# Optimization experiments

Measured on AMD Instinct MI355X. Metric: run time of the kernel, lower is better.

## Reference

```python
import jax, jax.numpy as jnp
import numpy as np

N_NODES = 100000
HIDDEN = 256
N_EDGES = 3200000


def _sage_conv(h, src, dst, Wl, bl, Wr, n_nodes):
    # PyG SAGEConv (aggr='mean', root_weight=True):
    #   out_i = Wl @ mean_{j in N(i)} h_j + bl + Wr @ h_i
    msgs = h[src]                                            # [E, D] gather
    summed = jax.ops.segment_sum(msgs, dst, num_segments=n_nodes)   # [N, D]
    deg = jax.ops.segment_sum(jnp.ones((src.shape[0],), h.dtype), dst,
                              num_segments=n_nodes)
    mean = summed / jnp.maximum(deg, 1.0)[:, None]
    return mean @ Wl.T + bl + h @ Wr.T


def _prelu(x, a):
    return jnp.where(x >= 0, x, a * x)


def setup_inputs() -> dict:
    key = jax.random.key(0)
    ks = jax.random.split(key, 16)
    D = HIDDEN
    s = 1.0 / np.sqrt(D)
    inp = {
        "x": jnp.arange(N_NODES, dtype=jnp.int64),
        "edge_index": jax.random.randint(ks[0], (2, N_EDGES), 0, N_NODES, dtype=jnp.int64),
        "edge_weight": jax.random.uniform(ks[1], (N_EDGES,), dtype=jnp.float32),
        "emb": jax.random.normal(ks[2], (N_NODES, D), dtype=jnp.float32),
    }
    i = 3
    for layer in (1, 2, 3):
        inp[f"Wl{layer}"] = jax.random.uniform(ks[i], (D, D), jnp.float32, -s, s); i += 1
        inp[f"bl{layer}"] = jax.random.uniform(ks[i], (D,), jnp.float32, -s, s); i += 1
        inp[f"Wr{layer}"] = jax.random.uniform(ks[i], (D, D), jnp.float32, -s, s); i += 1
        inp[f"a{layer}"] = jnp.array(0.25, jnp.float32)  # PReLU init
    inp["Wout"] = jax.random.uniform(ks[i], (D, D), jnp.float32, -s, s); i += 1
    inp["bout"] = jax.random.uniform(ks[i], (D,), jnp.float32, -s, s)
    return inp


def reference(x, edge_index, edge_weight, emb,
              Wl1, bl1, Wr1, a1,
              Wl2, bl2, Wr2, a2,
              Wl3, bl3, Wr3, a3,
              Wout, bout):
    # edge_weight is accepted but unused (original forward never passes it to SAGEConv).
    # Dropout treated as identity (eval mode) for a deterministic reference.
    n = emb.shape[0]
    src, dst = edge_index[0], edge_index[1]
    h0 = emb[x]                                              # embedding lookup
    h1 = _prelu(_sage_conv(h0, src, dst, Wl1, bl1, Wr1, n), a1)
    h2 = _prelu(_sage_conv(h1, src, dst, Wl2, bl2, Wr2, n), a2)
    h3 = _prelu(_sage_conv(h2, src, dst, Wl3, bl3, Wr3, n), a3)
    return h3 @ Wout.T + bout
```

## Files before the change

### kernel.cpp

```cpp
#include <hip/hip_runtime.h>

#define D 256
typedef unsigned short u16;
using short8  = __attribute__((ext_vector_type(8))) short;
using ushort8 = __attribute__((ext_vector_type(8))) unsigned short;
using f32x4   = __attribute__((ext_vector_type(4))) float;

#define BCHUNK  4096
#define FBINCAP 17500

__device__ __forceinline__ u16 f2bf(float f) {
    unsigned u = __float_as_uint(f);
    unsigned r = (u + 0x7FFFu + ((u >> 16) & 1u)) >> 16;
    return (u16)r;
}
__device__ __forceinline__ float bf2f(u16 v) {
    return __uint_as_float(((unsigned)v) << 16);
}

__device__ __forceinline__ void load_lds16(const u16* g, u16* l) {
    __builtin_amdgcn_global_load_lds(
        (const __attribute__((address_space(1))) void*)g,
        (__attribute__((address_space(3))) void*)l, 16, 0, 0);
}


__global__ void k_initcur(int* __restrict__ bincur, int nfbin) {
    int i = threadIdx.x;
    if (i < nfbin) bincur[i] = i * FBINCAP;
}

__global__ __launch_bounds__(256)
void k_binf(const int* __restrict__ src, const int* __restrict__ dst,
            int* __restrict__ bincur, unsigned* __restrict__ bins,
            int E, int nfbin) {
    __shared__ int cnt[256];
    __shared__ int bpos[256];
    int t = threadIdx.x;
    int base = blockIdx.x * BCHUNK;
    cnt[t] = 0;
    __syncthreads();
    int lim = E - base; if (lim > BCHUNK) lim = BCHUNK;
    for (int i = t; i < lim; i += 256)
        atomicAdd(&cnt[dst[base + i] >> 9], 1);
    __syncthreads();
    if (t < nfbin) {
        int c = cnt[t];
        bpos[t] = c > 0 ? atomicAdd(&bincur[t], c) : 0;
    }
    __syncthreads();
    cnt[t] = 0;
    __syncthreads();
    for (int i = t; i < lim; i += 256) {
        int d = dst[base + i], s = src[base + i];
        int fb = d >> 9;
        int r = atomicAdd(&cnt[fb], 1);
        bins[(size_t)bpos[fb] + r] = (unsigned)s | ((unsigned)(d & 511) << 17);
    }
}

__global__ __launch_bounds__(256)
void k_csrf(const unsigned* __restrict__ bins, const int* __restrict__ bincur,
            int* __restrict__ offs, int* __restrict__ ends,
            int* __restrict__ srcs, int N) {
    __shared__ int cnt[512];
    __shared__ int cur[512];
    __shared__ int ssum[256];
    __shared__ int loc[FBINCAP];
    int b = blockIdx.x, t = threadIdx.x;
    int bbase = b * FBINCAP;
    int ecnt = bincur[b] - bbase;
    cnt[t] = 0; cnt[t + 256] = 0;
    __syncthreads();
    const unsigned* bp = bins + bbase;
    for (int i = t; i < ecnt; i += 256)
        atomicAdd(&cnt[bp[i] >> 17], 1);
    __syncthreads();
    int a0 = cnt[2 * t], a1 = cnt[2 * t + 1];
    ssum[t] = a0 + a1;
    __syncthreads();
    for (int o = 1; o < 256; o <<= 1) {
        int x = (t >= o) ? ssum[t - o] : 0;
        __syncthreads();
        ssum[t] += x;
        __syncthreads();
    }
    int excl = ssum[t] - (a0 + a1);
    cur[2 * t] = excl;
    cur[2 * t + 1] = excl + a0;
    int nbase = b << 9;
    int l0 = nbase + 2 * t, l1 = l0 + 1;
    if (l0 < N) { offs[l0] = bbase + excl;      ends[l0] = bbase + excl + a0; }
    if (l1 < N) { offs[l1] = bbase + excl + a0; ends[l1] = bbase + excl + a0 + a1; }
    __syncthreads();
    for (int i = t; i < ecnt; i += 256) {
        unsigned v = bp[i];
        int p = atomicAdd(&cur[v >> 17], 1);
        loc[p] = (int)(v & 0x1FFFFu);
    }
    __syncthreads();
    for (int i = t; i < ecnt; i += 256)
        srcs[bbase + i] = loc[i];
}


__global__ void k_gather_bf(const int* __restrict__ x, const float* __restrict__ emb,
                            u16* __restrict__ h, int N) {
    int idx = blockIdx.x * blockDim.x + threadIdx.x;
    if (idx >= N * 64) return;
    int node = idx >> 6, c = idx & 63;
    int s = x[node];
    float4 v = ((const float4*)emb)[(size_t)s * 64 + c];
    ushort4 o;
    o.x = f2bf(v.x); o.y = f2bf(v.y); o.z = f2bf(v.z); o.w = f2bf(v.w);
    ((ushort4*)h)[(size_t)node * 64 + c] = o;
}


__global__ void k_cvtw(const float* w0, const float* w1, const float* w2,
                       const float* w3, const float* w4, const float* w5,
                       const float* w6, u16* __restrict__ out) {
    int idx = blockIdx.x * blockDim.x + threadIdx.x;
    if (idx >= 7 * 65536) return;
    int m = idx >> 16, off = idx & 65535;
    const float* w = w0;
    if (m == 1) w = w1; else if (m == 2) w = w2; else if (m == 3) w = w3;
    else if (m == 4) w = w4; else if (m == 5) w = w5; else if (m == 6) w = w6;
    out[idx] = f2bf(w[off]);
}


__global__ void k_agg_half(const u16* __restrict__ h, const int* __restrict__ offs,
                           const int* __restrict__ ends, const int* __restrict__ srcs,
                           u16* __restrict__ out, int colOff, int N) {
    int wid = (blockIdx.x * blockDim.x + threadIdx.x) >> 6;
    int lane = threadIdx.x & 63;
    if (wid >= N) return;
    int beg = offs[wid], end = ends[wid];
    int q = lane >> 4;
    int cl = lane & 15;
    const u16* hb = h + colOff + cl * 8;
    float acc[8];
    #pragma unroll
    for (int i = 0; i < 8; i++) acc[i] = 0.f;
    int e = beg + q;
    for (; e + 12 < end; e += 16) {
        int j0 = srcs[e], j1 = srcs[e + 4], j2 = srcs[e + 8], j3 = srcs[e + 12];
        ushort8 v0 = *(const ushort8*)&hb[(size_t)j0 * D];
        ushort8 v1 = *(const ushort8*)&hb[(size_t)j1 * D];
        ushort8 v2 = *(const ushort8*)&hb[(size_t)j2 * D];
        ushort8 v3 = *(const ushort8*)&hb[(size_t)j3 * D];
        #pragma unroll
        for (int i = 0; i < 8; i++)
            acc[i] += (bf2f(v0[i]) + bf2f(v1[i])) + (bf2f(v2[i]) + bf2f(v3[i]));
    }
    for (; e < end; e += 4) {
        int j = srcs[e];
        ushort8 v = *(const ushort8*)&hb[(size_t)j * D];
        #pragma unroll
        for (int i = 0; i < 8; i++) acc[i] += bf2f(v[i]);
    }
    #pragma unroll
    for (int i = 0; i < 8; i++) {
        acc[i] += __shfl_xor(acc[i], 16);
        acc[i] += __shfl_xor(acc[i], 32);
    }
    if (q == 0) {
        int dg = end - beg;
        float inv = 1.0f / (float)(dg < 1 ? 1 : dg);
        ushort8 o;
        #pragma unroll
        for (int i = 0; i < 8; i++) o[i] = f2bf(acc[i] * inv);
        *(ushort8*)&out[(size_t)wid * D + colOff + cl * 8] = o;
    }
}


__global__ __launch_bounds__(512)
void k_fgemm(const u16* __restrict__ A0, const u16* __restrict__ W0,
             const u16* __restrict__ A1, const u16* __restrict__ W1,
             int npairs,
             const float* __restrict__ bias, const float* __restrict__ prelu_a,
             void* __restrict__ outp, int out_bf16, int M) {
    __shared__ u16 As[128 * 32];
    __shared__ u16 Bs[256 * 32];
    int t = threadIdx.x;
    int wave = t >> 6, lane = t & 63;
    int r = lane & 15, quad = lane >> 4;
    int wm = (wave & 1) * 64;
    int wn = (wave >> 1) * 64;
    int m0 = blockIdx.x * 128;

    f32x4 acc[4][4];
    #pragma unroll
    for (int i = 0; i < 4; i++)
        #pragma unroll
        for (int j = 0; j < 4; j++)
            acc[i][j] = (f32x4){0.f, 0.f, 0.f, 0.f};

    int rowA  = t >> 2,           colA  = (t & 3) * 8;
    int rowB1 = (t + 512) >> 2;
    u16* ldsA  = &As[wave * 512];
    u16* ldsB0 = &Bs[wave * 512];
    u16* ldsB1 = &Bs[4096 + wave * 512];

    for (int p = 0; p < npairs; ++p) {
        const u16* Ag = p ? A1 : A0;
        const u16* Wg = p ? W1 : W0;
        for (int kt = 0; kt < 8; ++kt) {
            int k0 = kt * 32;
            __syncthreads();
            load_lds16(Ag + (size_t)(m0 + rowA) * D + k0 + colA, ldsA);
            load_lds16(Wg + (size_t)rowA * D + k0 + colA, ldsB0);
            load_lds16(Wg + (size_t)rowB1 * D + k0 + colA, ldsB1);
            __syncthreads();

            short8 a[4], b[4];
            #pragma unroll
            for (int mt = 0; mt < 4; mt++)
                a[mt] = *(const short8*)&As[(wm + mt * 16 + r) * 32 + quad * 8];
            #pragma unroll
            for (int nt = 0; nt < 4; nt++)
                b[nt] = *(const short8*)&Bs[(wn + nt * 16 + r) * 32 + quad * 8];
            #pragma unroll
            for (int mt = 0; mt < 4; mt++)
                #pragma unroll
                for (int nt = 0; nt < 4; nt++)
                    acc[mt][nt] = __builtin_amdgcn_mfma_f32_16x16x32_bf16(
                        a[mt], b[nt], acc[mt][nt], 0, 0, 0);
        }
    }

    float pa = prelu_a ? *prelu_a : 0.f;
    int dop = prelu_a != nullptr;
    #pragma unroll
    for (int nt = 0; nt < 4; nt++) {
        int col = wn + nt * 16 + r;
        float bv = bias ? bias[col] : 0.f;
        #pragma unroll
        for (int mt = 0; mt < 4; mt++) {
            #pragma unroll
            for (int i = 0; i < 4; i++) {
                int row = m0 + wm + mt * 16 + quad * 4 + i;
                if (row < M) {
                    float v = acc[mt][nt][i] + bv;
                    if (dop) v = (v >= 0.f) ? v : pa * v;
                    if (out_bf16)
                        ((u16*)outp)[(size_t)row * D + col] = f2bf(v);
                    else
                        ((float*)outp)[(size_t)row * D + col] = v;
                }
            }
        }
    }
}


extern "C" void kernel_launch(void* const* d_in, const int* in_sizes, int n_in,
                              void* d_out, int out_size, void* d_ws, size_t ws_size,
                              hipStream_t stream) {
    const int*   x    = (const int*)d_in[0];
    const int*   ei   = (const int*)d_in[1];
    const float* emb  = (const float*)d_in[3];
    const float* Wl[3] = {(const float*)d_in[4],  (const float*)d_in[8],  (const float*)d_in[12]};
    const float* bl[3] = {(const float*)d_in[5],  (const float*)d_in[9],  (const float*)d_in[13]};
    const float* Wr[3] = {(const float*)d_in[6],  (const float*)d_in[10], (const float*)d_in[14]};
    const float* pa[3] = {(const float*)d_in[7],  (const float*)d_in[11], (const float*)d_in[15]};
    const float* Wout = (const float*)d_in[16];
    const float* bout = (const float*)d_in[17];

    int N = in_sizes[0];
    int E = in_sizes[1] / 2;
    const int* src = ei;
    const int* dst = ei + E;
    int nfbin = (N + 511) >> 9;

    char* ws = (char*)d_ws;
    size_t off = 0;
    auto walloc = [&](size_t bytes) -> void* {
        void* p = ws + off;
        off += (bytes + 255) & ~(size_t)255;
        return p;
    };
    u16* hA   = (u16*)walloc((size_t)N * D * sizeof(u16));
    u16* hB   = (u16*)walloc((size_t)N * D * sizeof(u16));
    u16* mean = (u16*)walloc((size_t)N * D * sizeof(u16));
    u16* wbf  = (u16*)walloc((size_t)7 * 65536 * sizeof(u16));
    int* offs   = (int*)walloc((size_t)N * sizeof(int));
    int* ends   = (int*)walloc((size_t)N * sizeof(int));
    int* bincur = (int*)walloc(1024);
    unsigned* bins = (unsigned*)walloc((size_t)nfbin * FBINCAP * sizeof(unsigned));
    int* srcs   = (int*)walloc((size_t)nfbin * FBINCAP * sizeof(int));

    u16* Wlb[3] = {wbf + 0 * 65536, wbf + 2 * 65536, wbf + 4 * 65536};
    u16* Wrb[3] = {wbf + 1 * 65536, wbf + 3 * 65536, wbf + 5 * 65536};
    u16* Woutb  = wbf + 6 * 65536;

    k_cvtw<<<(7 * 65536 + 255) / 256, 256, 0, stream>>>(
        Wl[0], Wr[0], Wl[1], Wr[1], Wl[2], Wr[2], Wout, wbf);

    k_initcur<<<1, 256, 0, stream>>>(bincur, nfbin);
    int bb = (E + BCHUNK - 1) / BCHUNK;
    k_binf<<<bb, 256, 0, stream>>>(src, dst, bincur, bins, E, nfbin);
    k_csrf<<<nfbin, 256, 0, stream>>>(bins, bincur, offs, ends, srcs, N);

    k_gather_bf<<<(N * 64 + 255) / 256, 256, 0, stream>>>(x, emb, hA, N);

    int mb   = (N + 127) / 128;
    int aggb = (N + 3) / 4;

    k_agg_half<<<aggb, 256, 0, stream>>>(hA, offs, ends, srcs, mean, 0, N);
    k_agg_half<<<aggb, 256, 0, stream>>>(hA, offs, ends, srcs, mean, 128, N);
    k_fgemm<<<mb, 512, 0, stream>>>(mean, Wlb[0], hA, Wrb[0], 2, bl[0], pa[0], hB, 1, N);
    k_agg_half<<<aggb, 256, 0, stream>>>(hB, offs, ends, srcs, mean, 0, N);
    k_agg_half<<<aggb, 256, 0, stream>>>(hB, offs, ends, srcs, mean, 128, N);
    k_fgemm<<<mb, 512, 0, stream>>>(mean, Wlb[1], hB, Wrb[1], 2, bl[1], pa[1], hA, 1, N);
    k_agg_half<<<aggb, 256, 0, stream>>>(hA, offs, ends, srcs, mean, 0, N);
    k_agg_half<<<aggb, 256, 0, stream>>>(hA, offs, ends, srcs, mean, 128, N);
    k_fgemm<<<mb, 512, 0, stream>>>(mean, Wlb[2], hA, Wrb[2], 2, bl[2], pa[2], hB, 1, N);
    k_fgemm<<<mb, 512, 0, stream>>>(hB, Woutb, hB, Woutb, 1, bout, nullptr, d_out, 0, N);
}
```

Before: 1.159 ms.

## Merge half-column aggregation passes and double-buffer GEMM with swizzled LDS tiles

Measured after the change: 1.283 ms. 1.11x slower.

```diff
diff --git a/kernel.cpp b/kernel.cpp
--- a/kernel.cpp
+++ b/kernel.cpp
@@ -130,22 +130,23 @@
 }
 
 
-__global__ void k_agg_half(const u16* __restrict__ h, const int* __restrict__ offs,
-                           const int* __restrict__ ends, const int* __restrict__ srcs,
-                           u16* __restrict__ out, int colOff, int N) {
+__global__ __launch_bounds__(256)
+void k_agg(const u16* __restrict__ h, const int* __restrict__ offs,
+           const int* __restrict__ ends, const int* __restrict__ srcs,
+           u16* __restrict__ out, int N) {
     int wid = (blockIdx.x * blockDim.x + threadIdx.x) >> 6;
     int lane = threadIdx.x & 63;
     if (wid >= N) return;
     int beg = offs[wid], end = ends[wid];
-    int q = lane >> 4;
-    int cl = lane & 15;
-    const u16* hb = h + colOff + cl * 8;
+    int q = lane >> 5;
+    int cl = lane & 31;
+    const u16* hb = h + cl * 8;
     float acc[8];
     #pragma unroll
     for (int i = 0; i < 8; i++) acc[i] = 0.f;
     int e = beg + q;
-    for (; e + 12 < end; e += 16) {
-        int j0 = srcs[e], j1 = srcs[e + 4], j2 = srcs[e + 8], j3 = srcs[e + 12];
+    for (; e + 6 < end; e += 8) {
+        int j0 = srcs[e], j1 = srcs[e + 2], j2 = srcs[e + 4], j3 = srcs[e + 6];
         ushort8 v0 = *(const ushort8*)&hb[(size_t)j0 * D];
         ushort8 v1 = *(const ushort8*)&hb[(size_t)j1 * D];
         ushort8 v2 = *(const ushort8*)&hb[(size_t)j2 * D];
@@ -154,36 +155,33 @@
         for (int i = 0; i < 8; i++)
             acc[i] += (bf2f(v0[i]) + bf2f(v1[i])) + (bf2f(v2[i]) + bf2f(v3[i]));
     }
-    for (; e < end; e += 4) {
+    for (; e < end; e += 2) {
         int j = srcs[e];
         ushort8 v = *(const ushort8*)&hb[(size_t)j * D];
         #pragma unroll
         for (int i = 0; i < 8; i++) acc[i] += bf2f(v[i]);
     }
     #pragma unroll
-    for (int i = 0; i < 8; i++) {
-        acc[i] += __shfl_xor(acc[i], 16);
-        acc[i] += __shfl_xor(acc[i], 32);
-    }
+    for (int i = 0; i < 8; i++) acc[i] += __shfl_xor(acc[i], 32);
     if (q == 0) {
         int dg = end - beg;
         float inv = 1.0f / (float)(dg < 1 ? 1 : dg);
         ushort8 o;
         #pragma unroll
         for (int i = 0; i < 8; i++) o[i] = f2bf(acc[i] * inv);
-        *(ushort8*)&out[(size_t)wid * D + colOff + cl * 8] = o;
-    }
-}
-
-
-__global__ __launch_bounds__(512)
+        *(ushort8*)&out[(size_t)wid * D + cl * 8] = o;
+    }
+}
+
+
+__global__ __launch_bounds__(512, 2)
 void k_fgemm(const u16* __restrict__ A0, const u16* __restrict__ W0,
              const u16* __restrict__ A1, const u16* __restrict__ W1,
              int npairs,
              const float* __restrict__ bias, const float* __restrict__ prelu_a,
              void* __restrict__ outp, int out_bf16, int M) {
-    __shared__ u16 As[128 * 32];
-    __shared__ u16 Bs[256 * 32];
+    __shared__ u16 As[2][128 * 64];
+    __shared__ u16 Bs[2][256 * 64];
     int t = threadIdx.x;
     int wave = t >> 6, lane = t & 63;
     int r = lane & 15, quad = lane >> 4;
@@ -198,37 +196,68 @@
         for (int j = 0; j < 4; j++)
             acc[i][j] = (f32x4){0.f, 0.f, 0.f, 0.f};
 
-    int rowA  = t >> 2,           colA  = (t & 3) * 8;
-    int rowB1 = (t + 512) >> 2;
-    u16* ldsA  = &As[wave * 512];
-    u16* ldsB0 = &Bs[wave * 512];
-    u16* ldsB1 = &Bs[4096 + wave * 512];
-
-    for (int p = 0; p < npairs; ++p) {
-        const u16* Ag = p ? A1 : A0;
-        const u16* Wg = p ? W1 : W0;
-        for (int kt = 0; kt < 8; ++kt) {
-            int k0 = kt * 32;
-            __syncthreads();
-            load_lds16(Ag + (size_t)(m0 + rowA) * D + k0 + colA, ldsA);
-            load_lds16(Wg + (size_t)rowA * D + k0 + colA, ldsB0);
-            load_lds16(Wg + (size_t)rowB1 * D + k0 + colA, ldsB1);
-            __syncthreads();
-
-            short8 a[4], b[4];
+    int l8   = lane >> 3;
+    int cb   = (lane & 7) * 16;
+    int scol = (cb ^ (l8 << 4)) >> 1;
+    int arow = wave * 8 + l8;
+
+    int nkt = npairs * 4;
+
+    auto STAGE = [&](int buf, int kt) {
+        const u16* Ag = (kt >= 4) ? A1 : A0;
+        const u16* Wg = (kt >= 4) ? W1 : W0;
+        int k0 = (kt & 3) * 64;
+        #pragma unroll
+        for (int l = 0; l < 2; l++) {
+            int row = l * 64 + arow;
+            load_lds16(Ag + (size_t)(m0 + row) * D + k0 + scol,
+                       &As[buf][l * 4096 + wave * 512]);
+        }
+        #pragma unroll
+        for (int l = 0; l < 4; l++) {
+            int row = l * 64 + arow;
+            load_lds16(Wg + (size_t)row * D + k0 + scol,
+                       &Bs[buf][l * 4096 + wave * 512]);
+        }
+    };
+
+    STAGE(0, 0);
+    __syncthreads();
+
+    int cur = 0;
+    for (int kt = 0; kt < nkt; ++kt) {
+        if (kt + 1 < nkt) STAGE(cur ^ 1, kt + 1);
+
+        short8 a[2][4], b[2][4];
+        #pragma unroll
+        for (int ks = 0; ks < 2; ks++) {
             #pragma unroll
-            for (int mt = 0; mt < 4; mt++)
-                a[mt] = *(const short8*)&As[(wm + mt * 16 + r) * 32 + quad * 8];
+            for (int mt = 0; mt < 4; mt++) {
+                int row = wm + mt * 16 + r;
+                int col = (ks * 64 + quad * 16) ^ ((r & 7) << 4);
+                a[ks][mt] = *(const short8*)&As[cur][row * 64 + (col >> 1)];
+            }
             #pragma unroll
-            for (int nt = 0; nt < 4; nt++)
-                b[nt] = *(const short8*)&Bs[(wn + nt * 16 + r) * 32 + quad * 8];
+            for (int nt = 0; nt < 4; nt++) {
+                int row = wn + nt * 16 + r;
+                int col = (ks * 64 + quad * 16) ^ ((r & 7) << 4);
+                b[ks][nt] = *(const short8*)&Bs[cur][row * 64 + (col >> 1)];
+            }
+        }
+
+        __builtin_amdgcn_s_setprio(1);
+        #pragma unroll
+        for (int ks = 0; ks < 2; ks++)
             #pragma unroll
             for (int mt = 0; mt < 4; mt++)
                 #pragma unroll
                 for (int nt = 0; nt < 4; nt++)
                     acc[mt][nt] = __builtin_amdgcn_mfma_f32_16x16x32_bf16(
-                        a[mt], b[nt], acc[mt][nt], 0, 0, 0);
-        }
+                        a[ks][mt], b[ks][nt], acc[mt][nt], 0, 0, 0);
+        __builtin_amdgcn_s_setprio(0);
+
+        __syncthreads();
+        cur ^= 1;
     }
 
     float pa = prelu_a ? *prelu_a : 0.f;
@@ -307,16 +336,13 @@
     k_gather_bf<<<(N * 64 + 255) / 256, 256, 0, stream>>>(x, emb, hA, N);
 
     int mb   = (N + 127) / 128;
-    int aggb = (N + 3) / 4;
-
-    k_agg_half<<<aggb, 256, 0, stream>>>(hA, offs, ends, srcs, mean, 0, N);
-    k_agg_half<<<aggb, 256, 0, stream>>>(hA, offs, ends, srcs, mean, 128, N);
+    int aggb = (N * 64 + 255) / 256;
+
+    k_agg<<<aggb, 256, 0, stream>>>(hA, offs, ends, srcs, mean, N);
     k_fgemm<<<mb, 512, 0, stream>>>(mean, Wlb[0], hA, Wrb[0], 2, bl[0], pa[0], hB, 1, N);
-    k_agg_half<<<aggb, 256, 0, stream>>>(hB, offs, ends, srcs, mean, 0, N);
-    k_agg_half<<<aggb, 256, 0, stream>>>(hB, offs, ends, srcs, mean, 128, N);
+    k_agg<<<aggb, 256, 0, stream>>>(hB, offs, ends, srcs, mean, N);
     k_fgemm<<<mb, 512, 0, stream>>>(mean, Wlb[1], hB, Wrb[1], 2, bl[1], pa[1], hA, 1, N);
-    k_agg_half<<<aggb, 256, 0, stream>>>(hA, offs, ends, srcs, mean, 0, N);
-    k_agg_half<<<aggb, 256, 0, stream>>>(hA, offs, ends, srcs, mean, 128, N);
+    k_agg<<<aggb, 256, 0, stream>>>(hA, offs, ends, srcs, mean, N);
     k_fgemm<<<mb, 512, 0, stream>>>(mean, Wlb[2], hA, Wrb[2], 2, bl[2], pa[2], hB, 1, N);
     k_fgemm<<<mb, 512, 0, stream>>>(hB, Woutb, hB, Woutb, 1, bout, nullptr, d_out, 0, N);
 }
```

## Triple-buffer GEMM LDS loads with swizzle; split first-layer aggregation into quarters

Applied to the files above, without the earlier changes.

After: 1.179 ms. About the same (+1.7%).

```diff
diff --git a/kernel.cpp b/kernel.cpp
--- a/kernel.cpp
+++ b/kernel.cpp
@@ -130,9 +130,10 @@
 }
 
 
-__global__ void k_agg_half(const u16* __restrict__ h, const int* __restrict__ offs,
-                           const int* __restrict__ ends, const int* __restrict__ srcs,
-                           u16* __restrict__ out, int colOff, int N) {
+__global__ __launch_bounds__(256)
+void k_agg_h(const u16* __restrict__ h, const int* __restrict__ offs,
+             const int* __restrict__ ends, const int* __restrict__ srcs,
+             u16* __restrict__ out, int colOff, int N) {
     int wid = (blockIdx.x * blockDim.x + threadIdx.x) >> 6;
     int lane = threadIdx.x & 63;
     if (wid >= N) return;
@@ -176,14 +177,62 @@
 }
 
 
-__global__ __launch_bounds__(512)
+__global__ __launch_bounds__(256)
+void k_agg_q(const u16* __restrict__ h, const int* __restrict__ offs,
+             const int* __restrict__ ends, const int* __restrict__ srcs,
+             u16* __restrict__ out, int colOff, int N) {
+    int wid = (blockIdx.x * blockDim.x + threadIdx.x) >> 6;
+    int lane = threadIdx.x & 63;
+    if (wid >= N) return;
+    int beg = offs[wid], end = ends[wid];
+    int q = lane >> 3;
+    int cl = lane & 7;
+    const u16* hb = h + colOff + cl * 8;
+    float acc[8];
+    #pragma unroll
+    for (int i = 0; i < 8; i++) acc[i] = 0.f;
+    int e = beg + q;
+    for (; e + 24 < end; e += 32) {
+        int j0 = srcs[e], j1 = srcs[e + 8], j2 = srcs[e + 16], j3 = srcs[e + 24];
+        ushort8 v0 = *(const ushort8*)&hb[(size_t)j0 * D];
+        ushort8 v1 = *(const ushort8*)&hb[(size_t)j1 * D];
+        ushort8 v2 = *(const ushort8*)&hb[(size_t)j2 * D];
+        ushort8 v3 = *(const ushort8*)&hb[(size_t)j3 * D];
+        #pragma unroll
+        for (int i = 0; i < 8; i++)
+            acc[i] += (bf2f(v0[i]) + bf2f(v1[i])) + (bf2f(v2[i]) + bf2f(v3[i]));
+    }
+    for (; e < end; e += 8) {
+        int j = srcs[e];
+        ushort8 v = *(const ushort8*)&hb[(size_t)j * D];
+        #pragma unroll
+        for (int i = 0; i < 8; i++) acc[i] += bf2f(v[i]);
+    }
+    #pragma unroll
+    for (int i = 0; i < 8; i++) {
+        acc[i] += __shfl_xor(acc[i], 8);
+        acc[i] += __shfl_xor(acc[i], 16);
+        acc[i] += __shfl_xor(acc[i], 32);
+    }
+    if (q == 0) {
+        int dg = end - beg;
+        float inv = 1.0f / (float)(dg < 1 ? 1 : dg);
+        ushort8 o;
+        #pragma unroll
+        for (int i = 0; i < 8; i++) o[i] = f2bf(acc[i] * inv);
+        *(ushort8*)&out[(size_t)wid * D + colOff + cl * 8] = o;
+    }
+}
+
+
+__global__ __launch_bounds__(512, 4)
 void k_fgemm(const u16* __restrict__ A0, const u16* __restrict__ W0,
              const u16* __restrict__ A1, const u16* __restrict__ W1,
              int npairs,
              const float* __restrict__ bias, const float* __restrict__ prelu_a,
              void* __restrict__ outp, int out_bf16, int M) {
-    __shared__ u16 As[128 * 32];
-    __shared__ u16 Bs[256 * 32];
+    __shared__ u16 As[3][128 * 32];
+    __shared__ u16 Bs[3][256 * 32];
     int t = threadIdx.x;
     int wave = t >> 6, lane = t & 63;
     int r = lane & 15, quad = lane >> 4;
@@ -198,37 +247,54 @@
         for (int j = 0; j < 4; j++)
             acc[i][j] = (f32x4){0.f, 0.f, 0.f, 0.f};
 
-    int rowA  = t >> 2,           colA  = (t & 3) * 8;
-    int rowB1 = (t + 512) >> 2;
-    u16* ldsA  = &As[wave * 512];
-    u16* ldsB0 = &Bs[wave * 512];
-    u16* ldsB1 = &Bs[4096 + wave * 512];
-
-    for (int p = 0; p < npairs; ++p) {
-        const u16* Ag = p ? A1 : A0;
-        const u16* Wg = p ? W1 : W0;
-        for (int kt = 0; kt < 8; ++kt) {
-            int k0 = kt * 32;
-            __syncthreads();
-            load_lds16(Ag + (size_t)(m0 + rowA) * D + k0 + colA, ldsA);
-            load_lds16(Wg + (size_t)rowA * D + k0 + colA, ldsB0);
-            load_lds16(Wg + (size_t)rowB1 * D + k0 + colA, ldsB1);
-            __syncthreads();
-
-            short8 a[4], b[4];
-            #pragma unroll
-            for (int mt = 0; mt < 4; mt++)
-                a[mt] = *(const short8*)&As[(wm + mt * 16 + r) * 32 + quad * 8];
+    int arow = wave * 16 + (lane >> 2);
+    int scol = (((lane & 3) ^ ((lane >> 3) & 3)) << 3);
+    int nkt = npairs * 8;
+
+    auto STAGE = [&](int buf, int kt) {
+        const u16* Ag = (kt >= 8) ? A1 : A0;
+        const u16* Wg = (kt >= 8) ? W1 : W0;
+        int k0 = (kt & 7) * 32;
+        load_lds16(Ag + (size_t)(m0 + arow) * D + k0 + scol,
+                   &As[buf][wave * 512]);
+        #pragma unroll
+        for (int l = 0; l < 2; l++)
+            load_lds16(Wg + (size_t)(l * 128 + arow) * D + k0 + scol,
+                       &Bs[buf][l * 4096 + wave * 512]);
+    };
+
+    STAGE(0, 0);
+    if (nkt > 1) STAGE(1, 1);
+
+    int pch = quad ^ ((r >> 1) & 3);
+    int b0 = 0, b2 = 2;
+    for (int kt = 0; kt < nkt; ++kt) {
+        if (kt + 1 < nkt) asm volatile("s_waitcnt vmcnt(3)" ::: "memory");
+        else              asm volatile("s_waitcnt vmcnt(0)" ::: "memory");
+        __builtin_amdgcn_s_barrier();
+        asm volatile("" ::: "memory");
+
+        if (kt + 2 < nkt) STAGE(b2, kt + 2);
+
+        short8 a[4], b[4];
+        #pragma unroll
+        for (int mt = 0; mt < 4; mt++)
+            a[mt] = *(const short8*)&As[b0][(wm + mt * 16 + r) * 32 + pch * 8];
+        #pragma unroll
+        for (int nt = 0; nt < 4; nt++)
+            b[nt] = *(const short8*)&Bs[b0][(wn + nt * 16 + r) * 32 + pch * 8];
+
+        __builtin_amdgcn_s_setprio(1);
+        #pragma unroll
+        for (int mt = 0; mt < 4; mt++)
             #pragma unroll
             for (int nt = 0; nt < 4; nt++)
-                b[nt] = *(const short8*)&Bs[(wn + nt * 16 + r) * 32 + quad * 8];
-            #pragma unroll
-            for (int mt = 0; mt < 4; mt++)
-                #pragma unroll
-                for (int nt = 0; nt < 4; nt++)
-                    acc[mt][nt] = __builtin_amdgcn_mfma_f32_16x16x32_bf16(
-                        a[mt], b[nt], acc[mt][nt], 0, 0, 0);
-        }
+                acc[mt][nt] = __builtin_amdgcn_mfma_f32_16x16x32_bf16(
+                    a[mt], b[nt], acc[mt][nt], 0, 0, 0);
+        __builtin_amdgcn_s_setprio(0);
+
+        b0 = (b0 == 2) ? 0 : b0 + 1;
+        b2 = (b2 == 2) ? 0 : b2 + 1;
     }
 
     float pa = prelu_a ? *prelu_a : 0.f;
@@ -307,16 +373,18 @@
     k_gather_bf<<<(N * 64 + 255) / 256, 256, 0, stream>>>(x, emb, hA, N);
 
     int mb   = (N + 127) / 128;
-    int aggb = (N + 3) / 4;
-
-    k_agg_half<<<aggb, 256, 0, stream>>>(hA, offs, ends, srcs, mean, 0, N);
-    k_agg_half<<<aggb, 256, 0, stream>>>(hA, offs, ends, srcs, mean, 128, N);
+    int aggb = (N * 64 + 255) / 256;
+
+    k_agg_q<<<aggb, 256, 0, stream>>>(hA, offs, ends, srcs, mean, 0, N);
+    k_agg_q<<<aggb, 256, 0, stream>>>(hA, offs, ends, srcs, mean, 64, N);
+    k_agg_q<<<aggb, 256, 0, stream>>>(hA, offs, ends, srcs, mean, 128, N);
+    k_agg_q<<<aggb, 256, 0, stream>>>(hA, offs, ends, srcs, mean, 192, N);
     k_fgemm<<<mb, 512, 0, stream>>>(mean, Wlb[0], hA, Wrb[0], 2, bl[0], pa[0], hB, 1, N);
-    k_agg_half<<<aggb, 256, 0, stream>>>(hB, offs, ends, srcs, mean, 0, N);
-    k_agg_half<<<aggb, 256, 0, stream>>>(hB, offs, ends, srcs, mean, 128, N);
+    k_agg_h<<<aggb, 256, 0, stream>>>(hB, offs, ends, srcs, mean, 0, N);
+    k_agg_h<<<aggb, 256, 0, stream>>>(hB, offs, ends, srcs, mean, 128, N);
     k_fgemm<<<mb, 512, 0, stream>>>(mean, Wlb[1], hB, Wrb[1], 2, bl[1], pa[1], hA, 1, N);
-    k_agg_half<<<aggb, 256, 0, stream>>>(hA, offs, ends, srcs, mean, 0, N);
-    k_agg_half<<<aggb, 256, 0, stream>>>(hA, offs, ends, srcs, mean, 128, N);
+    k_agg_h<<<aggb, 256, 0, stream>>>(hA, offs, ends, srcs, mean, 0, N);
+    k_agg_h<<<aggb, 256, 0, stream>>>(hA, offs, ends, srcs, mean, 128, N);
     k_fgemm<<<mb, 512, 0, stream>>>(mean, Wlb[2], hA, Wrb[2], 2, bl[2], pa[2], hB, 1, N);
     k_fgemm<<<mb, 512, 0, stream>>>(hB, Woutb, hB, Woutb, 1, bout, nullptr, d_out, 0, N);
 }
```
